# Performance work log

Hardware: AMD Instinct MI355X
Metric: run time of the kernel (lower is better)

## Reference

```python
import jax, jax.numpy as jnp
import numpy as np
from math import sqrt

NUM_G = 32
N_HEADS = 8
D_MODEL = 512


def _linear(x, w, b):
    # torch nn.Linear: y = x @ W^T + b, W: (out, in)
    return jnp.einsum('...i,oi->...o', x, w) + b


def _full_attention(q, k, v):
    # q,k,v: [N, L, H, E]; no mask (mask_flag=False), dropout = identity (eval)
    E = q.shape[-1]
    scores = jnp.einsum('blhe,bshe->bhls', q, k)
    A = jax.nn.softmax(scores / sqrt(E), axis=-1)
    return jnp.einsum('bhls,bshd->blhd', A, v)


def setup_inputs() -> dict:
    key = jax.random.key(0)
    ks = jax.random.split(key, 15)
    B, ch, num_p, dim = 8, 1024, 8, D_MODEL
    x = jax.random.normal(ks[0], (B, ch, num_p, dim), dtype=jnp.float32)
    def lin(kw, kb):
        w = jax.random.normal(kw, (dim, dim), dtype=jnp.float32) * 0.02
        b = jax.random.normal(kb, (dim,), dtype=jnp.float32) * 0.02
        return w, b
    q1_w, q1_b = lin(ks[1], ks[2])
    k1_w, k1_b = lin(ks[3], ks[4])
    v1_w, v1_b = lin(ks[5], ks[6])
    q2_w, q2_b = lin(ks[7], ks[8])
    k2_w, k2_b = lin(ks[9], ks[10])
    v2_w, v2_b = lin(ks[11], ks[12])
    out_w, out_b = lin(ks[13], ks[14])
    return dict(x=x, q1_w=q1_w, q1_b=q1_b, k1_w=k1_w, k1_b=k1_b, v1_w=v1_w, v1_b=v1_b,
                q2_w=q2_w, q2_b=q2_b, k2_w=k2_w, k2_b=k2_b, v2_w=v2_w, v2_b=v2_b,
                out_w=out_w, out_b=out_b)


def reference(x, q1_w, q1_b, k1_w, k1_b, v1_w, v1_b,
              q2_w, q2_b, k2_w, k2_b, v2_w, v2_b, out_w, out_b):
    B, ch, num_p, dim = x.shape
    H, E = N_HEADS, dim // N_HEADS
    g = ch // NUM_G

    # 'B (num_g g) num_p p -> (B num_g num_p) g p'
    x1 = x.reshape(B, NUM_G, g, num_p, dim).transpose(0, 1, 3, 2, 4)
    x1 = x1.reshape(B * NUM_G * num_p, g, dim)

    # stage 1: inner-group attention over g
    q = _linear(x1, q1_w, q1_b).reshape(-1, g, H, E)
    k = _linear(x1, k1_w, k1_b).reshape(-1, g, H, E)
    v = _linear(x1, v1_w, v1_b).reshape(-1, g, H, E)
    y = _full_attention(q, k, v)  # [(B ng np), g, H, E]

    # '(B num_g num_p) g num_h p -> (B g num_p) num_g (num_h p)'
    y = y.reshape(B, NUM_G, num_p, g, H, E).transpose(0, 3, 2, 1, 4, 5)
    x2 = y.reshape(B * g * num_p, NUM_G, dim)

    # stage 2: inter-group attention over num_g
    q = _linear(x2, q2_w, q2_b).reshape(-1, NUM_G, H, E)
    k = _linear(x2, k2_w, k2_b).reshape(-1, NUM_G, H, E)
    v = _linear(x2, v2_w, v2_b).reshape(-1, NUM_G, H, E)
    y = _full_attention(q, k, v)  # [(B g np), num_g, H, E]

    # '(B g num_p) num_g num_h p -> B (num_g g) num_p (num_h p)'
    y = y.reshape(B, g, num_p, NUM_G, H, E).transpose(0, 3, 1, 2, 4, 5)
    y = y.reshape(B, ch, num_p, dim)

    return _linear(y, out_w, out_b)
```

## Files before the change

### kernel.cpp

```cpp
#include <hip/hip_runtime.h>
#include <hip/hip_bf16.h>

typedef __hip_bfloat16 bf16;
typedef __attribute__((ext_vector_type(8))) __bf16 bf16x8;
typedef __attribute__((ext_vector_type(4))) float f32x4;

__device__ __forceinline__ f32x4 mfma16(bf16x8 a, bf16x8 b, f32x4 c) {
  return __builtin_amdgcn_mfma_f32_16x16x32_bf16(a, b, c, 0, 0, 0);
}

__device__ __forceinline__ void gload_lds16(const void* g, void* lds) {
  __builtin_amdgcn_global_load_lds(
      (const __attribute__((address_space(1))) unsigned int*)g,
      (__attribute__((address_space(3))) unsigned int*)lds, 16, 0, 0);
}

__global__ __launch_bounds__(256)
void cvt_x_k(const float* __restrict__ s, bf16* __restrict__ d)
{
  const int i = (blockIdx.x * 256 + threadIdx.x) * 8;
  float4 a = *(const float4*)(s + i);
  float4 b = *(const float4*)(s + i + 4);
  union { bf16 h[8]; bf16x8 v; } u;
  u.h[0] = __float2bfloat16(a.x); u.h[1] = __float2bfloat16(a.y);
  u.h[2] = __float2bfloat16(a.z); u.h[3] = __float2bfloat16(a.w);
  u.h[4] = __float2bfloat16(b.x); u.h[5] = __float2bfloat16(b.y);
  u.h[6] = __float2bfloat16(b.z); u.h[7] = __float2bfloat16(b.w);
  *(bf16x8*)(d + i) = u.v;
}

__global__ __launch_bounds__(256)
void cvt_w_k(const float* s0, const float* s1, const float* s2, const float* s3,
             const float* s4, const float* s5, const float* s6, bf16* __restrict__ d)
{
  const int mat = blockIdx.x >> 7, blk = blockIdx.x & 127;
  const float* s;
  switch (mat) {
    case 0: s = s0; break; case 1: s = s1; break; case 2: s = s2; break;
    case 3: s = s3; break; case 4: s = s4; break; case 5: s = s5; break;
    default: s = s6; break;
  }
  const int i = (blk * 256 + threadIdx.x) * 8;
  float4 a = *(const float4*)(s + i);
  float4 b = *(const float4*)(s + i + 4);
  union { bf16 h[8]; bf16x8 v; } u;
  u.h[0] = __float2bfloat16(a.x); u.h[1] = __float2bfloat16(a.y);
  u.h[2] = __float2bfloat16(a.z); u.h[3] = __float2bfloat16(a.w);
  u.h[4] = __float2bfloat16(b.x); u.h[5] = __float2bfloat16(b.y);
  u.h[6] = __float2bfloat16(b.z); u.h[7] = __float2bfloat16(b.w);
  *(bf16x8*)(d + mat * 262144 + i) = u.v;
}

template<int MODE, int NBN>
__global__ __launch_bounds__(256)
void gemm_k(const bf16* __restrict__ A,
            const bf16* __restrict__ W0, const bf16* __restrict__ W1, const bf16* __restrict__ W2,
            const float* __restrict__ Bi0, const float* __restrict__ Bi1, const float* __restrict__ Bi2,
            bf16* __restrict__ O0, bf16* __restrict__ O1, bf16* __restrict__ O2,
            float* __restrict__ F0)
{
  __shared__ __align__(16) char smem[65536];
  bf16* const Ab0 = (bf16*)smem;
  bf16* const Ab1 = (bf16*)(smem + 16384);
  bf16* const Bb0 = (bf16*)(smem + 32768);
  bf16* const Bb1 = (bf16*)(smem + 49152);

  const int tid  = threadIdx.x;
  const int lane = tid & 63;
  const int w    = tid >> 6;

  const int per = gridDim.x >> 3;
  const int logical = (blockIdx.x & 7) * per + (blockIdx.x >> 3);
  const int bm = logical / NBN;
  const int bn = logical % NBN;
  const int m0 = bm * 128;
  const int n0 = bn * 128;

  const bf16* Wsel; const float* Bsel;
  int nbase;
  if (MODE == 0) { Wsel = W0; Bsel = Bi0; nbase = n0; }
  else {
    const int mat = n0 >> 9; nbase = n0 & 511;
    Wsel = (mat == 0) ? W0 : ((mat == 1) ? W1 : W2);
    Bsel = (mat == 0) ? Bi0 : ((mat == 1) ? Bi1 : Bi2);
  }

  const int lq = lane & 15, qd = lane >> 4;
  const int wr = (w >> 1) * 64, wc = (w & 1) * 64;
  const int sr    = lane >> 3;
  const int sslot = lane & 7;

  f32x4 acc[4][4];
#pragma unroll
  for (int i = 0; i < 4; ++i)
#pragma unroll
    for (int j = 0; j < 4; ++j) acc[i][j] = f32x4{0.f, 0.f, 0.f, 0.f};

  auto STAGE = [&](bf16* Abuf, bf16* Bbuf, int kt) {
#pragma unroll
    for (int j = 0; j < 4; ++j) {
      const int L0 = (w * 4 + j) * 1024;
      const int rr = (w * 4 + j) * 8 + sr;
      const int cb = kt * 128 + ((sslot ^ (rr & 7)) << 4);
      gload_lds16((const char*)A    + (size_t)(m0 + rr)    * 1024 + cb, (char*)Abuf + L0);
      gload_lds16((const char*)Wsel + (size_t)(nbase + rr) * 1024 + cb, (char*)Bbuf + L0);
    }
  };

  STAGE(Ab0, Bb0, 0);
  __syncthreads();

  for (int kt = 0; kt < 8; ++kt) {
    const bf16* Ac = (kt & 1) ? Ab1 : Ab0;
    const bf16* Bc = (kt & 1) ? Bb1 : Bb0;
    bf16* An = (kt & 1) ? Ab0 : Ab1;
    bf16* Bn = (kt & 1) ? Bb0 : Bb1;
    if (kt < 7) STAGE(An, Bn, kt + 1);

#pragma unroll
    for (int ks = 0; ks < 2; ++ks) {
      bf16x8 af[4], bfr[4];
#pragma unroll
      for (int mi = 0; mi < 4; ++mi) {
        const int row = wr + mi * 16 + lq;
        const int kb  = (ks * 64 + qd * 16) ^ ((row & 7) << 4);
        af[mi] = *(const bf16x8*)((const char*)Ac + row * 128 + kb);
      }
#pragma unroll
      for (int ni = 0; ni < 4; ++ni) {
        const int row = wc + ni * 16 + lq;
        const int kb  = (ks * 64 + qd * 16) ^ ((row & 7) << 4);
        bfr[ni] = *(const bf16x8*)((const char*)Bc + row * 128 + kb);
      }
      __builtin_amdgcn_s_setprio(1);
#pragma unroll
      for (int mi = 0; mi < 4; ++mi)
#pragma unroll
        for (int ni = 0; ni < 4; ++ni)
          acc[mi][ni] = mfma16(af[mi], bfr[ni], acc[mi][ni]);
      __builtin_amdgcn_s_setprio(0);
    }
    __syncthreads();
  }

  float biasv[4];
#pragma unroll
  for (int ni = 0; ni < 4; ++ni) {
    const int n = n0 + wc + ni * 16 + lq;
    const int nn = (MODE == 0) ? n : (n & 511);
    biasv[ni] = Bsel[nn];
  }

  if (MODE == 0) {
#pragma unroll
    for (int mi = 0; mi < 4; ++mi)
#pragma unroll
      for (int r = 0; r < 4; ++r) {
        const int m = m0 + wr + mi * 16 + qd * 4 + r;
#pragma unroll
        for (int ni = 0; ni < 4; ++ni)
          F0[(size_t)m * 512 + (n0 + wc + ni * 16 + lq)] = acc[mi][ni][r] + biasv[ni];
      }
  } else {
    bf16* const Ct = (bf16*)smem;
#pragma unroll
    for (int mi = 0; mi < 4; ++mi)
#pragma unroll
      for (int r = 0; r < 4; ++r) {
        const int row = wr + mi * 16 + qd * 4 + r;
#pragma unroll
        for (int ni = 0; ni < 4; ++ni)
          Ct[row * 136 + wc + ni * 16 + lq] = __float2bfloat16(acc[mi][ni][r] + biasv[ni]);
      }
    __syncthreads();

    const int mat = n0 >> 9;
    bf16* const Om = (mat == 0) ? O0 : ((mat == 1) ? O1 : O2);
    const int h0 = (n0 & 511) >> 6;
    const int sub = tid & 7;
#pragma unroll
    for (int p = 0; p < 8; ++p) {
      const int gid  = p * 32 + (tid >> 3);
      const int hsel = gid >> 7;
      const int mrow = gid & 127;
      const bf16x8 val = *(const bf16x8*)(Ct + mrow * 136 + hsel * 64 + sub * 8);
      const int m = m0 + mrow;
      int a, seq;
      if (MODE == 1) {
        const int b = m >> 13, c = (m >> 3) & 1023, pp = m & 7;
        a = (b * 32 + (c >> 5)) * 8 + pp;  seq = c & 31;
      } else {
        a = m >> 5;  seq = m & 31;
      }
      *(bf16x8*)(Om + ((size_t)((a * 8 + h0 + hsel) * 32 + seq)) * 64 + sub * 8) = val;
    }
  }
}

template<int STAGE>
__global__ __launch_bounds__(256)
void attn_k(const bf16* __restrict__ Q, const bf16* __restrict__ K,
            const bf16* __restrict__ V, bf16* __restrict__ Y)
{
  __shared__ __align__(16) char Plds[4][32 * 80];
  __shared__ __align__(16) char Vlds[4][32 * 132];
  const int tid  = threadIdx.x;
  const int lane = tid & 63;
  const int w    = tid >> 6;
  const int task = blockIdx.x * 4 + w;
  const int a = task >> 3, h = task & 7;
  const int lq = lane & 15, qd = lane >> 4;

  const bf16* Qb = Q + (size_t)(a * 8 + h) * 2048;
  const bf16* Kb = K + (size_t)(a * 8 + h) * 2048;
  const bf16* Vb = V + (size_t)(a * 8 + h) * 2048;

  {
    const int r  = lane >> 1;
    const int c0 = (lane & 1) * 32;
    union { bf16x8 v; unsigned u[4]; } t0, t1, t2, t3;
    t0.v = *(const bf16x8*)(Vb + r * 64 + c0);
    t1.v = *(const bf16x8*)(Vb + r * 64 + c0 + 8);
    t2.v = *(const bf16x8*)(Vb + r * 64 + c0 + 16);
    t3.v = *(const bf16x8*)(Vb + r * 64 + c0 + 24);
    unsigned* dst = (unsigned*)(Vlds[w] + r * 132 + c0 * 2);
#pragma unroll
    for (int j = 0; j < 4; ++j) dst[j]      = t0.u[j];
#pragma unroll
    for (int j = 0; j < 4; ++j) dst[4 + j]  = t1.u[j];
#pragma unroll
    for (int j = 0; j < 4; ++j) dst[8 + j]  = t2.u[j];
#pragma unroll
    for (int j = 0; j < 4; ++j) dst[12 + j] = t3.u[j];
  }

  bf16x8 qf[2][2], kf[2][2];
#pragma unroll
  for (int mi = 0; mi < 2; ++mi)
#pragma unroll
    for (int ks = 0; ks < 2; ++ks) {
      qf[mi][ks] = *(const bf16x8*)(Qb + (mi * 16 + lq) * 64 + ks * 32 + qd * 8);
      kf[mi][ks] = *(const bf16x8*)(Kb + (mi * 16 + lq) * 64 + ks * 32 + qd * 8);
    }

  f32x4 s[2][2];
#pragma unroll
  for (int mi = 0; mi < 2; ++mi)
#pragma unroll
    for (int ni = 0; ni < 2; ++ni) {
      s[mi][ni] = f32x4{0.f, 0.f, 0.f, 0.f};
#pragma unroll
      for (int ks = 0; ks < 2; ++ks)
        s[mi][ni] = mfma16(qf[mi][ks], kf[ni][ks], s[mi][ni]);
    }

  char* Pw = Plds[w];
  float rden[2][4];
#pragma unroll
  for (int mi = 0; mi < 2; ++mi) {
#pragma unroll
    for (int r = 0; r < 4; ++r) {
      float v0 = s[mi][0][r] * 0.125f, v1 = s[mi][1][r] * 0.125f;
      float mx = fmaxf(v0, v1);
#pragma unroll
      for (int d = 1; d < 16; d <<= 1) mx = fmaxf(mx, __shfl_xor(mx, d, 64));
      const float p0 = __expf(v0 - mx), p1 = __expf(v1 - mx);
      float sm = p0 + p1;
#pragma unroll
      for (int d = 1; d < 16; d <<= 1) sm += __shfl_xor(sm, d, 64);
      rden[mi][r] = 1.f / sm;
      const int qrow = mi * 16 + qd * 4 + r;
      bf16* prow = (bf16*)(Pw + qrow * 80);
      prow[lq]      = __float2bfloat16(p0);
      prow[16 + lq] = __float2bfloat16(p1);
    }
  }
  asm volatile("s_waitcnt lgkmcnt(0)" ::: "memory");
  __builtin_amdgcn_sched_barrier(0);

  bf16x8 pf[2];
#pragma unroll
  for (int mi = 0; mi < 2; ++mi)
    pf[mi] = *(const bf16x8*)(Pw + (mi * 16 + lq) * 80 + qd * 16);

  bf16x8 vf[4];
#pragma unroll
  for (int ni = 0; ni < 4; ++ni) {
    union { bf16 h[8]; bf16x8 v; } uv;
#pragma unroll
    for (int j = 0; j < 8; ++j)
      uv.h[j] = *(const bf16*)(Vlds[w] + (qd * 8 + j) * 132 + (ni * 16 + lq) * 2);
    vf[ni] = uv.v;
  }

  f32x4 o[2][4];
#pragma unroll
  for (int mi = 0; mi < 2; ++mi)
#pragma unroll
    for (int ni = 0; ni < 4; ++ni) {
      o[mi][ni] = f32x4{0.f, 0.f, 0.f, 0.f};
      o[mi][ni] = mfma16(pf[mi], vf[ni], o[mi][ni]);
    }

  int rowbase;
  if (STAGE == 1) { const int p = a & 7, ng = (a >> 3) & 31, b = a >> 8; rowbase = b * 8192 + p * 32 + ng; }
  else            { const int p = a & 7, i  = (a >> 3) & 31, b = a >> 8; rowbase = b * 8192 + i * 8 + p; }

#pragma unroll
  for (int mi = 0; mi < 2; ++mi) {
#pragma unroll
    for (int r = 0; r < 4; ++r) {
      const int q   = mi * 16 + qd * 4 + r;
      const int row = rowbase + q * 256;
      const float rd = rden[mi][r];
#pragma unroll
      for (int ni = 0; ni < 4; ++ni) {
        const int e = ni * 16 + lq;
        Y[(size_t)row * 512 + h * 64 + e] = __float2bfloat16(o[mi][ni][r] * rd);
      }
    }
  }
}

extern "C" void kernel_launch(void* const* d_in, const int* in_sizes, int n_in,
                              void* d_out, int out_size, void* d_ws, size_t ws_size,
                              hipStream_t stream) {
  const float* x   = (const float*)d_in[0];
  const float* q1w = (const float*)d_in[1];
  const float* q1b = (const float*)d_in[2];
  const float* k1w = (const float*)d_in[3];
  const float* k1b = (const float*)d_in[4];
  const float* v1w = (const float*)d_in[5];
  const float* v1b = (const float*)d_in[6];
  const float* q2w = (const float*)d_in[7];
  const float* q2b = (const float*)d_in[8];
  const float* k2w = (const float*)d_in[9];
  const float* k2b = (const float*)d_in[10];
  const float* v2w = (const float*)d_in[11];
  const float* v2b = (const float*)d_in[12];
  const float* ow  = (const float*)d_in[13];
  const float* ob  = (const float*)d_in[14];
  float* out = (float*)d_out;

  const size_t TOK = 65536ull * 512ull;
  const size_t WS1 = 262144;
  bf16* Xbf = (bf16*)d_ws;
  bf16* Qb  = Xbf + TOK;
  bf16* Kb  = Qb + TOK;
  bf16* Vb  = Kb + TOK;
  bf16* Wbf = Vb + TOK;
  bf16* X2  = Xbf;

  cvt_x_k<<<16384, 256, 0, stream>>>(x, Xbf);
  cvt_w_k<<<7 * 128, 256, 0, stream>>>(q1w, k1w, v1w, q2w, k2w, v2w, ow, Wbf);

  gemm_k<1, 12><<<512 * 12, 256, 0, stream>>>(Xbf, Wbf, Wbf + WS1, Wbf + 2 * WS1,
                                              q1b, k1b, v1b, Qb, Kb, Vb, nullptr);
  attn_k<1><<<4096, 256, 0, stream>>>(Qb, Kb, Vb, X2);
  gemm_k<2, 12><<<512 * 12, 256, 0, stream>>>(X2, Wbf + 3 * WS1, Wbf + 4 * WS1, Wbf + 5 * WS1,
                                              q2b, k2b, v2b, Qb, Kb, Vb, nullptr);
  attn_k<2><<<4096, 256, 0, stream>>>(Qb, Kb, Vb, X2);
  gemm_k<0, 4><<<512 * 4, 256, 0, stream>>>(X2, Wbf + 6 * WS1, Wbf + 6 * WS1, Wbf + 6 * WS1,
                                            ob, ob, ob, nullptr, nullptr, nullptr, out);
}
```

Before: 462.7 us.

## Replace GEMM with 256x256-tile 8-wave kernel using quarter-phase staged prefetch

Replaces the 128x128, 4-wave GEMM with a 256x256-tile, 512-thread kernel that uses 128 KB of LDS split into two stages. Each k-step is divided into four quadrant phases, and each phase issues a half-tile global-to-LDS load, synchronised with explicit vmcnt waits and barriers. The larger tile raises arithmetic intensity and the finer load schedule is meant to overlap memory with MFMA work. The epilogue is rewritten to use a swizzled LDS transpose. The cost is one block per CU, which lowers occupancy, and a small grid for the final projection (512 blocks).

```diff
diff --git a/kernel.cpp b/kernel.cpp
--- a/kernel.cpp
+++ b/kernel.cpp
@@ -52,147 +52,161 @@
 }
 
 template<int MODE, int NBN>
-__global__ __launch_bounds__(256)
-void gemm_k(const bf16* __restrict__ A,
-            const bf16* __restrict__ W0, const bf16* __restrict__ W1, const bf16* __restrict__ W2,
-            const float* __restrict__ Bi0, const float* __restrict__ Bi1, const float* __restrict__ Bi2,
-            bf16* __restrict__ O0, bf16* __restrict__ O1, bf16* __restrict__ O2,
-            float* __restrict__ F0)
+__global__ __launch_bounds__(512)
+void gemm2_k(const bf16* __restrict__ A,
+             const bf16* __restrict__ W0, const bf16* __restrict__ W1, const bf16* __restrict__ W2,
+             const float* __restrict__ Bi0, const float* __restrict__ Bi1, const float* __restrict__ Bi2,
+             bf16* __restrict__ O0, bf16* __restrict__ O1, bf16* __restrict__ O2,
+             float* __restrict__ F0)
 {
-  __shared__ __align__(16) char smem[65536];
-  bf16* const Ab0 = (bf16*)smem;
-  bf16* const Ab1 = (bf16*)(smem + 16384);
-  bf16* const Bb0 = (bf16*)(smem + 32768);
-  bf16* const Bb1 = (bf16*)(smem + 49152);
+  __shared__ __align__(16) char smem[131072];
 
   const int tid  = threadIdx.x;
   const int lane = tid & 63;
-  const int w    = tid >> 6;
+  const int wid  = tid >> 6;
+  const int wm   = wid >> 2;
+  const int wn   = wid & 3;
+  const int lq   = lane & 15, qd = lane >> 4;
 
   const int per = gridDim.x >> 3;
   const int logical = (blockIdx.x & 7) * per + (blockIdx.x >> 3);
   const int bm = logical / NBN;
   const int bn = logical % NBN;
-  const int m0 = bm * 128;
-  const int n0 = bn * 128;
-
-  const bf16* Wsel; const float* Bsel;
-  int nbase;
-  if (MODE == 0) { Wsel = W0; Bsel = Bi0; nbase = n0; }
+  const int m0 = bm * 256;
+  const int n0 = bn * 256;
+
+  const bf16* Wb; const float* Bsel; int nbase;
+  if (MODE == 0) { Wb = W0; Bsel = Bi0; nbase = n0; }
   else {
     const int mat = n0 >> 9; nbase = n0 & 511;
-    Wsel = (mat == 0) ? W0 : ((mat == 1) ? W1 : W2);
+    Wb   = (mat == 0) ? W0 : ((mat == 1) ? W1 : W2);
     Bsel = (mat == 0) ? Bi0 : ((mat == 1) ? Bi1 : Bi2);
   }
 
-  const int lq = lane & 15, qd = lane >> 4;
-  const int wr = (w >> 1) * 64, wc = (w & 1) * 64;
-  const int sr    = lane >> 3;
-  const int sslot = lane & 7;
-
-  f32x4 acc[4][4];
-#pragma unroll
-  for (int i = 0; i < 4; ++i)
+  f32x4 acc[8][4];
+#pragma unroll
+  for (int i = 0; i < 8; ++i)
 #pragma unroll
     for (int j = 0; j < 4; ++j) acc[i][j] = f32x4{0.f, 0.f, 0.f, 0.f};
 
-  auto STAGE = [&](bf16* Abuf, bf16* Bbuf, int kt) {
-#pragma unroll
-    for (int j = 0; j < 4; ++j) {
-      const int L0 = (w * 4 + j) * 1024;
-      const int rr = (w * 4 + j) * 8 + sr;
-      const int cb = kt * 128 + ((sslot ^ (rr & 7)) << 4);
-      gload_lds16((const char*)A    + (size_t)(m0 + rr)    * 1024 + cb, (char*)Abuf + L0);
-      gload_lds16((const char*)Wsel + (size_t)(nbase + rr) * 1024 + cb, (char*)Bbuf + L0);
+  auto stage_half = [&](int X, int h, int ktt, int tb) {
+#pragma unroll
+    for (int jj = 0; jj < 2; ++jj) {
+      const int id = wid * 2 + jj;
+      const int r  = id * 8 + (lane >> 3);
+      const int cb = ktt * 128 + (((lane & 7) ^ (r & 7)) << 4);
+      const char* g = X ? (const char*)Wb + (size_t)(nbase + h * 128 + r) * 1024 + cb
+                        : (const char*)A  + (size_t)(m0   + h * 128 + r) * 1024 + cb;
+      gload_lds16(g, smem + tb * 65536 + X * 32768 + h * 16384 + id * 1024);
     }
   };
 
-  STAGE(Ab0, Bb0, 0);
-  __syncthreads();
+#define GPHASE(QM, QN, SX, SH, KOFF) do {                                         \
+    const char* Ah = smem + bb + (QM) * 16384;                                    \
+    const char* Bh = smem + bb + 32768 + (QN) * 16384;                            \
+    bf16x8 af[4][2], bv[2][2];                                                    \
+    _Pragma("unroll") for (int i = 0; i < 4; ++i) {                               \
+      const int row = wm * 64 + i * 16 + lq;                                      \
+      _Pragma("unroll") for (int kk = 0; kk < 2; ++kk)                            \
+        af[i][kk] = *(const bf16x8*)(Ah + row * 128 + (((kk * 4 + qd) ^ (row & 7)) << 4)); \
+    }                                                                             \
+    _Pragma("unroll") for (int j = 0; j < 2; ++j) {                               \
+      const int row = wn * 32 + j * 16 + lq;                                      \
+      _Pragma("unroll") for (int kk = 0; kk < 2; ++kk)                            \
+        bv[j][kk] = *(const bf16x8*)(Bh + row * 128 + (((kk * 4 + qd) ^ (row & 7)) << 4)); \
+    }                                                                             \
+    stage_half((SX), (SH), (kt + (KOFF)) & 7, (kt + (KOFF)) & 1);                 \
+    __builtin_amdgcn_s_setprio(1);                                                \
+    _Pragma("unroll") for (int kk = 0; kk < 2; ++kk)                              \
+      _Pragma("unroll") for (int i = 0; i < 4; ++i)                               \
+        _Pragma("unroll") for (int j = 0; j < 2; ++j)                             \
+          acc[(QM) * 4 + i][(QN) * 2 + j] =                                       \
+              mfma16(af[i][kk], bv[j][kk], acc[(QM) * 4 + i][(QN) * 2 + j]);      \
+    __builtin_amdgcn_s_setprio(0);                                                \
+    asm volatile("s_waitcnt vmcnt(4)" ::: "memory");  \
+    __builtin_amdgcn_s_barrier();                     \
+    __builtin_amdgcn_sched_barrier(0);                \
+  } while (0)
+
+  stage_half(0, 0, 0, 0); stage_half(1, 0, 0, 0);
+  stage_half(1, 1, 0, 0); stage_half(0, 1, 0, 0);
+  stage_half(0, 0, 1, 1); stage_half(1, 1, 1, 1);
+  asm volatile("s_waitcnt vmcnt(4)" ::: "memory");
+  __builtin_amdgcn_s_barrier();
+  __builtin_amdgcn_sched_barrier(0);
 
   for (int kt = 0; kt < 8; ++kt) {
-    const bf16* Ac = (kt & 1) ? Ab1 : Ab0;
-    const bf16* Bc = (kt & 1) ? Bb1 : Bb0;
-    bf16* An = (kt & 1) ? Ab0 : Ab1;
-    bf16* Bn = (kt & 1) ? Bb0 : Bb1;
-    if (kt < 7) STAGE(An, Bn, kt + 1);
-
-#pragma unroll
-    for (int ks = 0; ks < 2; ++ks) {
-      bf16x8 af[4], bfr[4];
-#pragma unroll
-      for (int mi = 0; mi < 4; ++mi) {
-        const int row = wr + mi * 16 + lq;
-        const int kb  = (ks * 64 + qd * 16) ^ ((row & 7) << 4);
-        af[mi] = *(const bf16x8*)((const char*)Ac + row * 128 + kb);
-      }
-#pragma unroll
-      for (int ni = 0; ni < 4; ++ni) {
-        const int row = wc + ni * 16 + lq;
-        const int kb  = (ks * 64 + qd * 16) ^ ((row & 7) << 4);
-        bfr[ni] = *(const bf16x8*)((const char*)Bc + row * 128 + kb);
-      }
-      __builtin_amdgcn_s_setprio(1);
-#pragma unroll
-      for (int mi = 0; mi < 4; ++mi)
-#pragma unroll
-        for (int ni = 0; ni < 4; ++ni)
-          acc[mi][ni] = mfma16(af[mi], bfr[ni], acc[mi][ni]);
-      __builtin_amdgcn_s_setprio(0);
-    }
-    __syncthreads();
-  }
+    const int bb = (kt & 1) * 65536;
+    GPHASE(0, 0, 0, 1, 1);
+    GPHASE(0, 1, 1, 0, 1);
+    GPHASE(1, 1, 0, 0, 2);
+    GPHASE(1, 0, 1, 1, 2);
+  }
+#undef GPHASE
+
+  asm volatile("s_waitcnt vmcnt(0)" ::: "memory");
+  __builtin_amdgcn_s_barrier();
+  __builtin_amdgcn_sched_barrier(0);
 
   float biasv[4];
 #pragma unroll
   for (int ni = 0; ni < 4; ++ni) {
-    const int n = n0 + wc + ni * 16 + lq;
-    const int nn = (MODE == 0) ? n : (n & 511);
-    biasv[ni] = Bsel[nn];
+    const int col = (ni >> 1) * 128 + wn * 32 + (ni & 1) * 16 + lq;
+    biasv[ni] = Bsel[(MODE == 0) ? (n0 + col) : (nbase + col)];
   }
 
   if (MODE == 0) {
 #pragma unroll
-    for (int mi = 0; mi < 4; ++mi)
+    for (int mi = 0; mi < 8; ++mi)
 #pragma unroll
       for (int r = 0; r < 4; ++r) {
-        const int m = m0 + wr + mi * 16 + qd * 4 + r;
-#pragma unroll
-        for (int ni = 0; ni < 4; ++ni)
-          F0[(size_t)m * 512 + (n0 + wc + ni * 16 + lq)] = acc[mi][ni][r] + biasv[ni];
+        const int m = m0 + (mi >> 2) * 128 + wm * 64 + (mi & 3) * 16 + qd * 4 + r;
+#pragma unroll
+        for (int ni = 0; ni < 4; ++ni) {
+          const int n = n0 + (ni >> 1) * 128 + wn * 32 + (ni & 1) * 16 + lq;
+          F0[(size_t)m * 512 + n] = acc[mi][ni][r] + biasv[ni];
+        }
       }
   } else {
-    bf16* const Ct = (bf16*)smem;
-#pragma unroll
-    for (int mi = 0; mi < 4; ++mi)
-#pragma unroll
-      for (int r = 0; r < 4; ++r) {
-        const int row = wr + mi * 16 + qd * 4 + r;
-#pragma unroll
-        for (int ni = 0; ni < 4; ++ni)
-          Ct[row * 136 + wc + ni * 16 + lq] = __float2bfloat16(acc[mi][ni][r] + biasv[ni]);
-      }
-    __syncthreads();
-
     const int mat = n0 >> 9;
     bf16* const Om = (mat == 0) ? O0 : ((mat == 1) ? O1 : O2);
     const int h0 = (n0 & 511) >> 6;
-    const int sub = tid & 7;
-#pragma unroll
-    for (int p = 0; p < 8; ++p) {
-      const int gid  = p * 32 + (tid >> 3);
-      const int hsel = gid >> 7;
-      const int mrow = gid & 127;
-      const bf16x8 val = *(const bf16x8*)(Ct + mrow * 136 + hsel * 64 + sub * 8);
-      const int m = m0 + mrow;
-      int a, seq;
-      if (MODE == 1) {
-        const int b = m >> 13, c = (m >> 3) & 1023, pp = m & 7;
-        a = (b * 32 + (c >> 5)) * 8 + pp;  seq = c & 31;
-      } else {
-        a = m >> 5;  seq = m & 31;
+#pragma unroll
+    for (int qm = 0; qm < 2; ++qm) {
+#pragma unroll
+      for (int i = 0; i < 4; ++i)
+#pragma unroll
+        for (int r = 0; r < 4; ++r) {
+          const int row = wm * 64 + i * 16 + qd * 4 + r;
+          const int sw  = (row & 7) ^ (((row >> 3) & 3) << 3);
+#pragma unroll
+          for (int ni = 0; ni < 4; ++ni) {
+            const int col  = (ni >> 1) * 128 + wn * 32 + (ni & 1) * 16 + lq;
+            const int byte = row * 512 + (((col >> 3) ^ sw) << 4) + (col & 7) * 2;
+            *(bf16*)(smem + byte) = __float2bfloat16(acc[qm * 4 + i][ni][r] + biasv[ni]);
+          }
+        }
+      __syncthreads();
+      {
+        const int hh   = tid >> 7;
+        const int mrow = tid & 127;
+        const int m    = m0 + qm * 128 + mrow;
+        int a, seq;
+        if (MODE == 1) {
+          const int b = m >> 13, c = (m >> 3) & 1023, pp = m & 7;
+          a = (b * 32 + (c >> 5)) * 8 + pp;  seq = c & 31;
+        } else {
+          a = m >> 5;  seq = m & 31;
+        }
+        const int sw = (mrow & 7) ^ (((mrow >> 3) & 3) << 3);
+        bf16* const dst = Om + ((size_t)((a * 8 + h0 + hh) * 32 + seq)) * 64;
+#pragma unroll
+        for (int j = 0; j < 8; ++j) {
+          const bf16x8 v = *(const bf16x8*)(smem + mrow * 512 + (((hh * 8 + j) ^ sw) << 4));
+          *(bf16x8*)(dst + j * 8) = v;
+        }
       }
-      *(bf16x8*)(Om + ((size_t)((a * 8 + h0 + hsel) * 32 + seq)) * 64 + sub * 8) = val;
+      __syncthreads();
     }
   }
 }
@@ -354,12 +368,12 @@
   cvt_x_k<<<16384, 256, 0, stream>>>(x, Xbf);
   cvt_w_k<<<7 * 128, 256, 0, stream>>>(q1w, k1w, v1w, q2w, k2w, v2w, ow, Wbf);
 
-  gemm_k<1, 12><<<512 * 12, 256, 0, stream>>>(Xbf, Wbf, Wbf + WS1, Wbf + 2 * WS1,
-                                              q1b, k1b, v1b, Qb, Kb, Vb, nullptr);
+  gemm2_k<1, 6><<<1536, 512, 0, stream>>>(Xbf, Wbf, Wbf + WS1, Wbf + 2 * WS1,
+                                          q1b, k1b, v1b, Qb, Kb, Vb, nullptr);
   attn_k<1><<<4096, 256, 0, stream>>>(Qb, Kb, Vb, X2);
-  gemm_k<2, 12><<<512 * 12, 256, 0, stream>>>(X2, Wbf + 3 * WS1, Wbf + 4 * WS1, Wbf + 5 * WS1,
-                                              q2b, k2b, v2b, Qb, Kb, Vb, nullptr);
+  gemm2_k<2, 6><<<1536, 512, 0, stream>>>(X2, Wbf + 3 * WS1, Wbf + 4 * WS1, Wbf + 5 * WS1,
+                                          q2b, k2b, v2b, Qb, Kb, Vb, nullptr);
   attn_k<2><<<4096, 256, 0, stream>>>(Qb, Kb, Vb, X2);
-  gemm_k<0, 4><<<512 * 4, 256, 0, stream>>>(X2, Wbf + 6 * WS1, Wbf + 6 * WS1, Wbf + 6 * WS1,
-                                            ob, ob, ob, nullptr, nullptr, nullptr, out);
-}
+  gemm2_k<0, 2><<<512, 512, 0, stream>>>(X2, Wbf + 6 * WS1, Wbf + 6 * WS1, Wbf + 6 * WS1,
+                                         ob, ob, ob, nullptr, nullptr, nullptr, out);
+}
```

After: 519.4 us. +12.3%, slower.

## Halve GEMM K-tile to cut LDS use and raise occupancy

Applied to the files above, without the earlier changes.

Shrinks the GEMM K tile from 64 to 32 elements, so the double-buffered shared memory drops from 64KB to 32KB and the kernel runs 16 K-steps instead of 8. The swizzle is adapted to 64-byte rows, a min-blocks launch bound is added, and the bf16 epilogue is split into two 64-row halves so the staging buffer fits in the smaller shared array. The goal is more resident blocks per CU to hide memory latency, paid for with twice as many barriers per tile and more serialized epilogue passes.

```diff
diff --git a/kernel.cpp b/kernel.cpp
--- a/kernel.cpp
+++ b/kernel.cpp
@@ -52,18 +52,18 @@
 }
 
 template<int MODE, int NBN>
-__global__ __launch_bounds__(256)
+__global__ __launch_bounds__(256, 5)
 void gemm_k(const bf16* __restrict__ A,
             const bf16* __restrict__ W0, const bf16* __restrict__ W1, const bf16* __restrict__ W2,
             const float* __restrict__ Bi0, const float* __restrict__ Bi1, const float* __restrict__ Bi2,
             bf16* __restrict__ O0, bf16* __restrict__ O1, bf16* __restrict__ O2,
             float* __restrict__ F0)
 {
-  __shared__ __align__(16) char smem[65536];
-  bf16* const Ab0 = (bf16*)smem;
-  bf16* const Ab1 = (bf16*)(smem + 16384);
-  bf16* const Bb0 = (bf16*)(smem + 32768);
-  bf16* const Bb1 = (bf16*)(smem + 49152);
+  __shared__ __align__(16) char smem[32768];
+  char* const Ab0 = smem;
+  char* const Ab1 = smem + 8192;
+  char* const Bb0 = smem + 16384;
+  char* const Bb1 = smem + 24576;
 
   const int tid  = threadIdx.x;
   const int lane = tid & 63;
@@ -87,8 +87,8 @@
 
   const int lq = lane & 15, qd = lane >> 4;
   const int wr = (w >> 1) * 64, wc = (w & 1) * 64;
-  const int sr    = lane >> 3;
-  const int sslot = lane & 7;
+  const int srow  = lane >> 2;
+  const int sslot = lane & 3;
 
   f32x4 acc[4][4];
 #pragma unroll
@@ -96,50 +96,45 @@
 #pragma unroll
     for (int j = 0; j < 4; ++j) acc[i][j] = f32x4{0.f, 0.f, 0.f, 0.f};
 
-  auto STAGE = [&](bf16* Abuf, bf16* Bbuf, int kt) {
-#pragma unroll
-    for (int j = 0; j < 4; ++j) {
-      const int L0 = (w * 4 + j) * 1024;
-      const int rr = (w * 4 + j) * 8 + sr;
-      const int cb = kt * 128 + ((sslot ^ (rr & 7)) << 4);
-      gload_lds16((const char*)A    + (size_t)(m0 + rr)    * 1024 + cb, (char*)Abuf + L0);
-      gload_lds16((const char*)Wsel + (size_t)(nbase + rr) * 1024 + cb, (char*)Bbuf + L0);
+  auto STAGE = [&](char* Abuf, char* Bbuf, int kt) {
+#pragma unroll
+    for (int j = 0; j < 2; ++j) {
+      const int id = w * 2 + j;
+      const int rr = id * 16 + srow;
+      const int cb = kt * 64 + ((sslot ^ (rr & 3)) << 4);
+      gload_lds16((const char*)A    + (size_t)(m0 + rr)    * 1024 + cb, Abuf + id * 1024);
+      gload_lds16((const char*)Wsel + (size_t)(nbase + rr) * 1024 + cb, Bbuf + id * 1024);
     }
   };
 
   STAGE(Ab0, Bb0, 0);
   __syncthreads();
 
-  for (int kt = 0; kt < 8; ++kt) {
-    const bf16* Ac = (kt & 1) ? Ab1 : Ab0;
-    const bf16* Bc = (kt & 1) ? Bb1 : Bb0;
-    bf16* An = (kt & 1) ? Ab0 : Ab1;
-    bf16* Bn = (kt & 1) ? Bb0 : Bb1;
-    if (kt < 7) STAGE(An, Bn, kt + 1);
-
-#pragma unroll
-    for (int ks = 0; ks < 2; ++ks) {
-      bf16x8 af[4], bfr[4];
-#pragma unroll
-      for (int mi = 0; mi < 4; ++mi) {
-        const int row = wr + mi * 16 + lq;
-        const int kb  = (ks * 64 + qd * 16) ^ ((row & 7) << 4);
-        af[mi] = *(const bf16x8*)((const char*)Ac + row * 128 + kb);
-      }
-#pragma unroll
-      for (int ni = 0; ni < 4; ++ni) {
-        const int row = wc + ni * 16 + lq;
-        const int kb  = (ks * 64 + qd * 16) ^ ((row & 7) << 4);
-        bfr[ni] = *(const bf16x8*)((const char*)Bc + row * 128 + kb);
-      }
-      __builtin_amdgcn_s_setprio(1);
-#pragma unroll
-      for (int mi = 0; mi < 4; ++mi)
-#pragma unroll
-        for (int ni = 0; ni < 4; ++ni)
-          acc[mi][ni] = mfma16(af[mi], bfr[ni], acc[mi][ni]);
-      __builtin_amdgcn_s_setprio(0);
-    }
+  for (int kt = 0; kt < 16; ++kt) {
+    const char* Ac = (kt & 1) ? Ab1 : Ab0;
+    const char* Bc = (kt & 1) ? Bb1 : Bb0;
+    char* An = (kt & 1) ? Ab0 : Ab1;
+    char* Bn = (kt & 1) ? Bb0 : Bb1;
+    if (kt < 15) STAGE(An, Bn, kt + 1);
+
+    bf16x8 af[4], bfr[4];
+#pragma unroll
+    for (int mi = 0; mi < 4; ++mi) {
+      const int row = wr + mi * 16 + lq;
+      af[mi] = *(const bf16x8*)(Ac + row * 64 + ((qd ^ (row & 3)) << 4));
+    }
+#pragma unroll
+    for (int ni = 0; ni < 4; ++ni) {
+      const int row = wc + ni * 16 + lq;
+      bfr[ni] = *(const bf16x8*)(Bc + row * 64 + ((qd ^ (row & 3)) << 4));
+    }
+    __builtin_amdgcn_s_setprio(1);
+#pragma unroll
+    for (int mi = 0; mi < 4; ++mi)
+#pragma unroll
+      for (int ni = 0; ni < 4; ++ni)
+        acc[mi][ni] = mfma16(af[mi], bfr[ni], acc[mi][ni]);
+    __builtin_amdgcn_s_setprio(0);
     __syncthreads();
   }
 
@@ -163,36 +158,42 @@
       }
   } else {
     bf16* const Ct = (bf16*)smem;
-#pragma unroll
-    for (int mi = 0; mi < 4; ++mi)
-#pragma unroll
-      for (int r = 0; r < 4; ++r) {
-        const int row = wr + mi * 16 + qd * 4 + r;
-#pragma unroll
-        for (int ni = 0; ni < 4; ++ni)
-          Ct[row * 136 + wc + ni * 16 + lq] = __float2bfloat16(acc[mi][ni][r] + biasv[ni]);
-      }
-    __syncthreads();
-
     const int mat = n0 >> 9;
     bf16* const Om = (mat == 0) ? O0 : ((mat == 1) ? O1 : O2);
     const int h0 = (n0 & 511) >> 6;
-    const int sub = tid & 7;
-#pragma unroll
-    for (int p = 0; p < 8; ++p) {
-      const int gid  = p * 32 + (tid >> 3);
-      const int hsel = gid >> 7;
-      const int mrow = gid & 127;
-      const bf16x8 val = *(const bf16x8*)(Ct + mrow * 136 + hsel * 64 + sub * 8);
-      const int m = m0 + mrow;
-      int a, seq;
-      if (MODE == 1) {
-        const int b = m >> 13, c = (m >> 3) & 1023, pp = m & 7;
-        a = (b * 32 + (c >> 5)) * 8 + pp;  seq = c & 31;
-      } else {
-        a = m >> 5;  seq = m & 31;
+#pragma unroll
+    for (int h2 = 0; h2 < 2; ++h2) {
+      if ((w >> 1) == h2) {
+#pragma unroll
+        for (int mi = 0; mi < 4; ++mi)
+#pragma unroll
+          for (int r = 0; r < 4; ++r) {
+            const int lrow = mi * 16 + qd * 4 + r;
+#pragma unroll
+            for (int ni = 0; ni < 4; ++ni)
+              Ct[lrow * 136 + wc + ni * 16 + lq] = __float2bfloat16(acc[mi][ni][r] + biasv[ni]);
+          }
       }
-      *(bf16x8*)(Om + ((size_t)((a * 8 + h0 + hsel) * 32 + seq)) * 64 + sub * 8) = val;
+      __syncthreads();
+#pragma unroll
+      for (int p = 0; p < 4; ++p) {
+        const int c    = p * 256 + tid;
+        const int mrow = c & 63;
+        const int hcol = c >> 6;
+        const int hsel = hcol >> 3;
+        const int sub  = hcol & 7;
+        const bf16x8 val = *(const bf16x8*)(Ct + mrow * 136 + hsel * 64 + sub * 8);
+        const int m = m0 + h2 * 64 + mrow;
+        int a, seq;
+        if (MODE == 1) {
+          const int b = m >> 13, cc = (m >> 3) & 1023, pp = m & 7;
+          a = (b * 32 + (cc >> 5)) * 8 + pp;  seq = cc & 31;
+        } else {
+          a = m >> 5;  seq = m & 31;
+        }
+        *(bf16x8*)(Om + ((size_t)((a * 8 + h0 + hsel) * 32 + seq)) * 64 + sub * 8) = val;
+      }
+      __syncthreads();
     }
   }
 }
```

Measured after the change: 1.470 ms. 3.18x slower.
